# Kernel tuning notes

Measured on AMD Instinct MI355X. Metric: run time of the kernel, lower is better.

## Reference

```python
import jax, jax.numpy as jnp
import numpy as np

N_NODES = 50000
N_EDGES = 800000
D_IN = 128
D_HID = 128
D_OUT = 64
N_CONV = 4  # num_layers=5 -> 4 GINConv layers
BN_EPS = 1e-5


def setup_inputs() -> dict:
    key = jax.random.key(0)
    ks = jax.random.split(key, 16)
    h = jax.random.normal(ks[0], (N_NODES, D_IN), dtype=jnp.float32)
    src = jax.random.randint(ks[1], (N_EDGES,), 0, N_NODES)
    dst = jax.random.randint(ks[2], (N_EDGES,), 0, N_NODES)
    s = 0.05
    return {
        "h": h, "src": src, "dst": dst,
        # MLP inside each GINConv: Linear(no bias) -> BN -> ReLU -> Linear(no bias)
        "W1": jax.random.normal(ks[3], (N_CONV, D_IN, D_HID), dtype=jnp.float32) * s,
        "W2": jax.random.normal(ks[4], (N_CONV, D_HID, D_HID), dtype=jnp.float32) * s,
        "bn1_g": jnp.ones((N_CONV, D_HID), jnp.float32),
        "bn1_b": jnp.zeros((N_CONV, D_HID), jnp.float32),
        # outer BatchNorm after each GINConv
        "bn2_g": jnp.ones((N_CONV, D_HID), jnp.float32),
        "bn2_b": jnp.zeros((N_CONV, D_HID), jnp.float32),
        # 5 linear_prediction heads (layer 0 acts on input features)
        "pred_W": jax.random.normal(ks[5], (N_CONV + 1, D_HID, D_OUT), dtype=jnp.float32) * s,
        "pred_b": jnp.zeros((N_CONV + 1, D_OUT), jnp.float32),
    }


def _batchnorm(x, gamma, beta):
    # training-mode BatchNorm1d: batch statistics over the node dimension
    m = jnp.mean(x, axis=0)
    v = jnp.var(x, axis=0)
    return (x - m) * jax.lax.rsqrt(v + BN_EPS) * gamma + beta


def reference(h, src, dst, W1, W2, bn1_g, bn1_b, bn2_g, bn2_b, pred_W, pred_b):
    hidden_rep = [h]
    for i in range(N_CONV):
        # GINConv, learn_eps=False (eps=0): (1+eps)*h + sum of neighbor features
        agg = jax.ops.segment_sum(h[src], dst, num_segments=N_NODES)
        z = h + agg
        # MLP: Linear -> BN -> ReLU -> Linear
        z = z @ W1[i]
        z = jax.nn.relu(_batchnorm(z, bn1_g[i], bn1_b[i]))
        z = z @ W2[i]
        # outer BN + ReLU
        h = jax.nn.relu(_batchnorm(z, bn2_g[i], bn2_b[i]))
        hidden_rep.append(h)
    # SumPooling over the single graph, per-layer prediction heads (dropout = identity at eval)
    score = jnp.zeros((D_OUT,), h.dtype)
    for i, hr in enumerate(hidden_rep):
        pooled = jnp.sum(hr, axis=0)  # [D]
        score = score + pooled @ pred_W[i] + pred_b[i]
    return score  # [D_OUT], matches .view(shape[1])
```

## Files before the change

### kernel.cpp

```cpp
#include <hip/hip_runtime.h>
#include <hip/hip_bf16.h>

#define N_NODES 50000
#define N_EDGES 800000
#define D 128

typedef __bf16 bf16;
typedef __attribute__((ext_vector_type(8))) __bf16 bf16x8;
typedef __attribute__((ext_vector_type(4))) __bf16 bf16x4;
typedef __attribute__((ext_vector_type(16))) float f32x16;
typedef _Float16 f16;
typedef __attribute__((ext_vector_type(2))) _Float16 f16x2;
typedef __attribute__((ext_vector_type(4))) _Float16 f16x4;
typedef __attribute__((ext_vector_type(8))) _Float16 f16x8;

__global__ __launch_bounds__(256)
void initprep_kernel(const float* __restrict__ W1, const float* __restrict__ W2,
                     bf16* __restrict__ WfH, bf16* __restrict__ WfL,
                     int* __restrict__ deg, float* __restrict__ stats,
                     float* __restrict__ ppart, float* __restrict__ pooled,
                     int* __restrict__ done) {
    int b = blockIdx.x, t = threadIdx.x;
    if (b < 64) {
        int gid = b * 256 + t;
        int lane = gid & 63;
        int grp = gid >> 6;
        int sub = grp & 7;
        int cf = (grp >> 3) & 3;
        int m = grp >> 5;
        const float* Wsrc = (m < 4) ? (W1 + m * 16384) : (W2 + (m - 4) * 16384);
        int col = cf * 32 + (lane & 31);
        int kb = sub * 16 + 8 * (lane >> 5);
        bf16x8 h, l;
#pragma unroll
        for (int j = 0; j < 8; ++j) {
            float w = Wsrc[(kb + j) * 128 + col];
            bf16 hb = (bf16)w;
            bf16 lb = (bf16)(w - (float)hb);
            h[j] = hb;
            l[j] = lb;
        }
        int idx = m * 16384 + ((grp & 31) * 64 + lane) * 8;
        *(bf16x8*)&WfH[idx] = h;
        *(bf16x8*)&WfL[idx] = l;
    } else {
        int i = (b - 64) * 256 + t;
        if (i < N_NODES) deg[i] = 0;
        if (i < 2048) stats[i] = 0.f;
        if (i < 24576) ppart[i] = 0.f;
        if (i < 640) pooled[i] = 0.f;
        if (i < 2) done[i] = 0;
    }
}

__global__ void hist_kernel(const int* __restrict__ dst, int* __restrict__ deg) {
    int e = blockIdx.x * 256 + threadIdx.x;
    atomicAdd(&deg[dst[e]], 1);
}

__global__ __launch_bounds__(256)
void scanAB_kernel(const int* __restrict__ deg, int* __restrict__ bsum,
                   int* __restrict__ boff, int* __restrict__ done) {
    __shared__ int red[256];
    __shared__ int lastflag;
    int t = threadIdx.x;
    int g = blockIdx.x * 256 + t;
    red[t] = (g < N_NODES) ? deg[g] : 0;
    __syncthreads();
    for (int off = 128; off > 0; off >>= 1) {
        if (t < off) red[t] += red[t + off];
        __syncthreads();
    }
    if (t == 0) {
        __hip_atomic_store(&bsum[blockIdx.x], red[0], __ATOMIC_RELEASE,
                           __HIP_MEMORY_SCOPE_AGENT);
        __threadfence();
        int v = atomicAdd(&done[0], 1);
        lastflag = (v == (int)gridDim.x - 1);
    }
    __syncthreads();
    if (!lastflag) return;
    __shared__ int s[256];
    int v = (t < 196) ? __hip_atomic_load(&bsum[t], __ATOMIC_ACQUIRE,
                                          __HIP_MEMORY_SCOPE_AGENT)
                      : 0;
    s[t] = v;
    __syncthreads();
    for (int off = 1; off < 256; off <<= 1) {
        int a = (t >= off) ? s[t - off] : 0;
        __syncthreads();
        s[t] += a;
        __syncthreads();
    }
    boff[t] = (t == 0) ? 0 : s[t - 1];
}

__global__ __launch_bounds__(256)
void scanC_kernel(const int* __restrict__ deg, const int* __restrict__ boff,
                  int* __restrict__ row_start, int* __restrict__ cursor) {
    __shared__ int s[256];
    int t = threadIdx.x;
    int g = blockIdx.x * 256 + t;
    int v = (g < N_NODES) ? deg[g] : 0;
    s[t] = v;
    __syncthreads();
    for (int off = 1; off < 256; off <<= 1) {
        int a = (t >= off) ? s[t - off] : 0;
        __syncthreads();
        s[t] += a;
        __syncthreads();
    }
    int excl = boff[blockIdx.x] + s[t] - v;
    if (g < N_NODES) {
        row_start[g] = excl;
        cursor[g] = excl;
    }
    if (blockIdx.x == 0 && t == 0) row_start[N_NODES] = N_EDGES;
}

__global__ void fill_kernel(const int* __restrict__ src, const int* __restrict__ dst,
                            int* __restrict__ cursor, int* __restrict__ esrc) {
    int e = blockIdx.x * 256 + threadIdx.x;
    int d = dst[e];
    int p = atomicAdd(&cursor[d], 1);
    esrc[p] = src[e];
}

__global__ __launch_bounds__(256)
void conv0_kernel(const float* __restrict__ Y, f16* __restrict__ Hb,
                  float* __restrict__ pooled) {
    __shared__ float red[8][128];
    int t = threadIdx.x;
    int c = (t & 31) << 2;
    int rrow = t >> 5;
    float4 p = make_float4(0.f, 0.f, 0.f, 0.f);
    for (int r = blockIdx.x * 8 + rrow; r < N_NODES; r += gridDim.x * 8) {
        float4 v = *(const float4*)&Y[r * D + c];
        f16x4 h4;
        h4[0] = (f16)v.x; h4[1] = (f16)v.y; h4[2] = (f16)v.z; h4[3] = (f16)v.w;
        *(f16x4*)&Hb[r * D + c] = h4;
        p.x += v.x; p.y += v.y; p.z += v.z; p.w += v.w;
    }
    *(float4*)&red[rrow][c] = p;
    __syncthreads();
    if (t < 128) {
        float s = 0.f;
#pragma unroll
        for (int i = 0; i < 8; ++i) s += red[i][t];
        atomicAdd(&pooled[t], s);
    }
}

template <bool APPLY>
__global__ __launch_bounds__(256)
void agg_kernel(const f16* __restrict__ H, const int* __restrict__ esrc,
                const int* __restrict__ row_start, const float* __restrict__ stats,
                const float* __restrict__ gam, const float* __restrict__ bet,
                f16* __restrict__ Z, float* __restrict__ ppart) {
    __shared__ float sred[4][128];
    int wv = threadIdx.x >> 6;
    int v = blockIdx.x * 4 + wv;
    int lane = threadIdx.x & 63;
    int c2 = lane << 1;
    float a0 = 1.f, b0 = 0.f, a1 = 1.f, b1 = 0.f;
    if (APPLY) {
        float m0 = stats[c2] * (1.0f / N_NODES);
        float q0 = stats[128 + c2] * (1.0f / N_NODES);
        float g0 = gam[c2] * rsqrtf(q0 - m0 * m0 + 1e-5f);
        a0 = g0; b0 = bet[c2] - m0 * g0;
        float m1 = stats[c2 + 1] * (1.0f / N_NODES);
        float q1 = stats[128 + c2 + 1] * (1.0f / N_NODES);
        float g1 = gam[c2 + 1] * rsqrtf(q1 - m1 * m1 + 1e-5f);
        a1 = g1; b1 = bet[c2 + 1] - m1 * g1;
    }
    int beg = row_start[v], end_ = row_start[v + 1];
    f16x2 sv = *(const f16x2*)&H[v * D + c2];
    float ax = (float)sv[0], ay = (float)sv[1];
    if (APPLY) {
        ax = fmaxf(fmaf(a0, ax, b0), 0.f);
        ay = fmaxf(fmaf(a1, ay, b1), 0.f);
        sred[wv][c2] = ax;
        sred[wv][c2 + 1] = ay;
    }
    int e = beg;
    for (; e + 4 <= end_; e += 4) {
        int s0 = esrc[e], s1 = esrc[e + 1], s2 = esrc[e + 2], s3 = esrc[e + 3];
        f16x2 v0 = *(const f16x2*)&H[s0 * D + c2];
        f16x2 v1 = *(const f16x2*)&H[s1 * D + c2];
        f16x2 v2 = *(const f16x2*)&H[s2 * D + c2];
        f16x2 v3 = *(const f16x2*)&H[s3 * D + c2];
        if (APPLY) {
            ax += fmaxf(fmaf(a0, (float)v0[0], b0), 0.f) + fmaxf(fmaf(a0, (float)v1[0], b0), 0.f)
                + fmaxf(fmaf(a0, (float)v2[0], b0), 0.f) + fmaxf(fmaf(a0, (float)v3[0], b0), 0.f);
            ay += fmaxf(fmaf(a1, (float)v0[1], b1), 0.f) + fmaxf(fmaf(a1, (float)v1[1], b1), 0.f)
                + fmaxf(fmaf(a1, (float)v2[1], b1), 0.f) + fmaxf(fmaf(a1, (float)v3[1], b1), 0.f);
        } else {
            ax += (float)v0[0] + (float)v1[0] + (float)v2[0] + (float)v3[0];
            ay += (float)v0[1] + (float)v1[1] + (float)v2[1] + (float)v3[1];
        }
    }
    for (; e < end_; ++e) {
        int s0 = esrc[e];
        f16x2 v0 = *(const f16x2*)&H[s0 * D + c2];
        if (APPLY) {
            ax += fmaxf(fmaf(a0, (float)v0[0], b0), 0.f);
            ay += fmaxf(fmaf(a1, (float)v0[1], b1), 0.f);
        } else {
            ax += (float)v0[0];
            ay += (float)v0[1];
        }
    }
    f16x2 zv;
    zv[0] = (f16)ax;
    zv[1] = (f16)ay;
    *(f16x2*)&Z[v * D + c2] = zv;
    if (APPLY) {
        __syncthreads();
        int t = threadIdx.x;
        if (t < 128) {
            float s = sred[0][t] + sred[1][t] + sred[2][t] + sred[3][t];
            atomicAdd(&ppart[(blockIdx.x & 63) * 128 + t], s);
        }
    }
}

template <bool BN_IN>
__global__ __launch_bounds__(256, 2)
void mm_kernel(const f16* __restrict__ X, const bf16* __restrict__ WfH,
               const bf16* __restrict__ WfL, const float* __restrict__ stats_in,
               const float* __restrict__ gam, const float* __restrict__ bet,
               f16* __restrict__ Y, float* __restrict__ stats_out) {
    __shared__ bf16 Ah[4096];
    __shared__ bf16 Al[4096];
    __shared__ float ab[2][128];

    int t = threadIdx.x;
    int w = t >> 6, lane = t & 63;
    if (BN_IN && t < 128) {
        float s = stats_in[t] * (1.0f / N_NODES);
        float q = stats_in[128 + t] * (1.0f / N_NODES);
        float a = gam[t] * rsqrtf(q - s * s + 1e-5f);
        ab[0][t] = a;
        ab[1][t] = bet[t] - s * a;
    }

    bf16x8 Bh[8], Bl[8];
#pragma unroll
    for (int c = 0; c < 8; ++c) {
        int idx = ((w * 8 + c) * 64 + lane) * 8;
        Bh[c] = *(const bf16x8*)&WfH[idx];
        Bl[c] = *(const bf16x8*)&WfL[idx];
    }

    f32x16 acc[4];
#pragma unroll
    for (int fr = 0; fr < 4; ++fr) acc[fr] = (f32x16)0.0f;

    int rowbase = blockIdx.x * 128;
    int nrows = min(128, N_NODES - rowbase);
    int srow = t >> 1;
    int sk0 = (t & 1) * 16;
    __syncthreads();

    for (int kb = 0; kb < 4; ++kb) {
        if (kb) __syncthreads();
        {
            float vf[16];
#pragma unroll
            for (int j = 0; j < 16; ++j) vf[j] = 0.f;
            if (srow < nrows) {
                const f16* xr = &X[(rowbase + srow) * D + kb * 32 + sk0];
                f16x8 u0 = *(const f16x8*)&xr[0];
                f16x8 u1 = *(const f16x8*)&xr[8];
#pragma unroll
                for (int j = 0; j < 8; ++j) {
                    vf[j] = (float)u0[j];
                    vf[8 + j] = (float)u1[j];
                }
                if (BN_IN) {
#pragma unroll
                    for (int j = 0; j < 16; ++j) {
                        int kg = kb * 32 + sk0 + j;
                        vf[j] = fmaxf(fmaf(ab[0][kg], vf[j], ab[1][kg]), 0.f);
                    }
                }
            }
#pragma unroll
            for (int i = 0; i < 4; ++i) {
                bf16x4 h4, l4;
#pragma unroll
                for (int j = 0; j < 4; ++j) {
                    bf16 hb = (bf16)vf[i * 4 + j];
                    h4[j] = hb;
                    l4[j] = (bf16)(vf[i * 4 + j] - (float)hb);
                }
                int e = srow * 32 + sk0 + i * 4;
                int es = e ^ ((srow & 7) << 3);
                *(bf16x4*)&Ah[es] = h4;
                *(bf16x4*)&Al[es] = l4;
            }
        }
        __syncthreads();
#pragma unroll
        for (int s2 = 0; s2 < 2; ++s2) {
            int sg = kb * 2 + s2;
#pragma unroll
            for (int fr = 0; fr < 4; ++fr) {
                int row = fr * 32 + (lane & 31);
                int e = row * 32 + s2 * 16 + 8 * (lane >> 5);
                int es = e ^ ((row & 7) << 3);
                bf16x8 ah = *(const bf16x8*)&Ah[es];
                bf16x8 al = *(const bf16x8*)&Al[es];
                acc[fr] = __builtin_amdgcn_mfma_f32_32x32x16_bf16(al, Bh[sg], acc[fr], 0, 0, 0);
                acc[fr] = __builtin_amdgcn_mfma_f32_32x32x16_bf16(ah, Bl[sg], acc[fr], 0, 0, 0);
                acc[fr] = __builtin_amdgcn_mfma_f32_32x32x16_bf16(ah, Bh[sg], acc[fr], 0, 0, 0);
            }
        }
    }

    int col = w * 32 + (lane & 31);
    float psum = 0.f, psq = 0.f;
#pragma unroll
    for (int fr = 0; fr < 4; ++fr) {
#pragma unroll
        for (int r = 0; r < 16; ++r) {
            float v = acc[fr][r];
            int row = fr * 32 + (r & 3) + 8 * (r >> 2) + 4 * (lane >> 5);
            if (row < nrows) Y[(rowbase + row) * D + col] = (f16)v;
            psum += v;
            psq += v * v;
        }
    }
    psum += __shfl_xor(psum, 32);
    psq += __shfl_xor(psq, 32);
    if (lane < 32) {
        atomicAdd(&stats_out[col], psum);
        atomicAdd(&stats_out[128 + col], psq);
    }
}

__global__ __launch_bounds__(256)
void pool4head_kernel(const f16* __restrict__ Y, const float* __restrict__ stats,
                      const float* __restrict__ gam, const float* __restrict__ bet,
                      float* __restrict__ pooled, const float* __restrict__ ppart,
                      const float* __restrict__ pW, const float* __restrict__ pB,
                      float* __restrict__ out, int* __restrict__ done) {
    __shared__ float abS[2][128];
    __shared__ float red[8][128];
    __shared__ int lastflag;
    int t = threadIdx.x;
    if (t < 128) {
        float s = stats[t] * (1.0f / N_NODES);
        float q = stats[128 + t] * (1.0f / N_NODES);
        float a = gam[t] * rsqrtf(q - s * s + 1e-5f);
        abS[0][t] = a;
        abS[1][t] = bet[t] - s * a;
    }
    __syncthreads();
    int c = (t & 31) << 2;
    int rrow = t >> 5;
    float4 A = *(const float4*)&abS[0][c];
    float4 B = *(const float4*)&abS[1][c];
    float4 p = make_float4(0.f, 0.f, 0.f, 0.f);
    for (int r = blockIdx.x * 8 + rrow; r < N_NODES; r += gridDim.x * 8) {
        f16x4 v = *(const f16x4*)&Y[r * D + c];
        p.x += fmaxf(fmaf(A.x, (float)v[0], B.x), 0.f);
        p.y += fmaxf(fmaf(A.y, (float)v[1], B.y), 0.f);
        p.z += fmaxf(fmaf(A.z, (float)v[2], B.z), 0.f);
        p.w += fmaxf(fmaf(A.w, (float)v[3], B.w), 0.f);
    }
    *(float4*)&red[rrow][c] = p;
    __syncthreads();
    if (t < 128) {
        float s = 0.f;
#pragma unroll
        for (int i = 0; i < 8; ++i) s += red[i][t];
        atomicAdd(&pooled[512 + t], s);
    }
    __syncthreads();
    if (t == 0) {
        __threadfence();
        int v = atomicAdd(&done[1], 1);
        lastflag = (v == (int)gridDim.x - 1);
    }
    __syncthreads();
    if (!lastflag) return;

    __shared__ float pl[5][128];
    if (t < 128) {
        pl[0][t] = pooled[t];
        for (int l = 1; l <= 3; ++l) {
            float s = 0.f;
            for (int sl = 0; sl < 64; ++sl) s += ppart[(l - 1) * 8192 + sl * 128 + t];
            pl[l][t] = s;
        }
        pl[4][t] = __hip_atomic_load(&pooled[512 + t], __ATOMIC_ACQUIRE,
                                     __HIP_MEMORY_SCOPE_AGENT);
    }
    __syncthreads();
    if (t < 64) {
        float acc = 0.f;
        for (int l = 0; l < 5; ++l) {
            acc += pB[l * 64 + t];
            const float* wp = pW + l * 8192;
            const float* pp = pl[l];
            for (int cc = 0; cc < 128; ++cc) acc += pp[cc] * wp[cc * 64 + t];
        }
        out[t] = acc;
    }
}

extern "C" void kernel_launch(void* const* d_in, const int* in_sizes, int n_in,
                              void* d_out, int out_size, void* d_ws, size_t ws_size,
                              hipStream_t stream) {
    const float* h0 = (const float*)d_in[0];
    const int* src = (const int*)d_in[1];
    const int* dst = (const int*)d_in[2];
    const float* W1 = (const float*)d_in[3];
    const float* W2 = (const float*)d_in[4];
    const float* bn1_g = (const float*)d_in[5];
    const float* bn1_b = (const float*)d_in[6];
    const float* bn2_g = (const float*)d_in[7];
    const float* bn2_b = (const float*)d_in[8];
    const float* pW = (const float*)d_in[9];
    const float* pB = (const float*)d_in[10];
    float* out = (float*)d_out;

    char* ws = (char*)d_ws;
    f16* B0 = (f16*)(ws + 0);
    f16* B1 = (f16*)(ws + 12800000);
    f16* B2 = (f16*)(ws + 25600000);
    int* esrc = (int*)(ws + 38400000);
    int* deg = (int*)(ws + 54412288);
    int* row_start = (int*)(ws + 54612288);
    int* cursor = (int*)(ws + 54812304);
    int* done = (int*)(ws + 55012304);
    int* bsum = (int*)(ws + 55015440);
    int* boff = (int*)(ws + 55016224);
    float* stats = (float*)(ws + 55017248);
    float* ppart = (float*)(ws + 55025440);
    float* pooled = (float*)(ws + 55123744);
    bf16* WfH = (bf16*)(ws + 55126304);
    bf16* WfL = (bf16*)(ws + 55388448);

    initprep_kernel<<<260, 256, 0, stream>>>(W1, W2, WfH, WfL, deg, stats, ppart, pooled,
                                             done);
    hist_kernel<<<3125, 256, 0, stream>>>(dst, deg);
    scanAB_kernel<<<196, 256, 0, stream>>>(deg, bsum, boff, done);
    scanC_kernel<<<196, 256, 0, stream>>>(deg, boff, row_start, cursor);
    fill_kernel<<<3125, 256, 0, stream>>>(src, dst, cursor, esrc);
    conv0_kernel<<<512, 256, 0, stream>>>(h0, B0, pooled);

    for (int i = 0; i < 4; ++i) {
        if (i == 0) {
            agg_kernel<false><<<12500, 256, 0, stream>>>(B0, esrc, row_start, nullptr,
                                                         nullptr, nullptr, B1, nullptr);
        } else {
            agg_kernel<true><<<12500, 256, 0, stream>>>(
                B0, esrc, row_start, stats + (4 + i - 1) * 256, bn2_g + (i - 1) * 128,
                bn2_b + (i - 1) * 128, B1, ppart + (i - 1) * 8192);
        }
        mm_kernel<false><<<391, 256, 0, stream>>>(B1, WfH + i * 16384, WfL + i * 16384,
                                                  nullptr, nullptr, nullptr, B2,
                                                  stats + i * 256);
        mm_kernel<true><<<391, 256, 0, stream>>>(B2, WfH + (4 + i) * 16384,
                                                 WfL + (4 + i) * 16384, stats + i * 256,
                                                 bn1_g + i * 128, bn1_b + i * 128, B0,
                                                 stats + (4 + i) * 256);
    }
    pool4head_kernel<<<512, 256, 0, stream>>>(B0, stats + 7 * 256, bn2_g + 3 * 128,
                                              bn2_b + 3 * 128, pooled, ppart, pW, pB, out,
                                              done);
}
```

Before: 594.2 us.

## Fuse conv0 into init, single-pass lookback scan, parallelize pooling head

Moves the fp32-to-fp16 input conversion into the init kernel and folds layer-0 pooling into the first aggregation kernel. The two-kernel degree scan is replaced by a single-pass scan where each block spins on predecessor flags. The final pooled-partial reduction is spread over several blocks and the prediction-head matvec uses all 256 threads. The aim is fewer launches and a shorter serial tail, at the risk of spin-wait dependence on block residency.

```diff
diff --git a/kernel.cpp b/kernel.cpp
--- a/kernel.cpp
+++ b/kernel.cpp
@@ -18,8 +18,10 @@
 void initprep_kernel(const float* __restrict__ W1, const float* __restrict__ W2,
                      bf16* __restrict__ WfH, bf16* __restrict__ WfL,
                      int* __restrict__ deg, float* __restrict__ stats,
-                     float* __restrict__ ppart, float* __restrict__ pooled,
-                     int* __restrict__ done) {
+                     float* __restrict__ ppart, float* __restrict__ plglob,
+                     float* __restrict__ pooled4, int* __restrict__ done,
+                     int* __restrict__ flags, const float* __restrict__ h0,
+                     f16* __restrict__ Hb) {
     int b = blockIdx.x, t = threadIdx.x;
     if (b < 64) {
         int gid = b * 256 + t;
@@ -43,13 +45,24 @@
         int idx = m * 16384 + ((grp & 31) * 64 + lane) * 8;
         *(bf16x8*)&WfH[idx] = h;
         *(bf16x8*)&WfL[idx] = l;
-    } else {
+    } else if (b < 260) {
         int i = (b - 64) * 256 + t;
         if (i < N_NODES) deg[i] = 0;
         if (i < 2048) stats[i] = 0.f;
-        if (i < 24576) ppart[i] = 0.f;
-        if (i < 640) pooled[i] = 0.f;
+        if (i < 32768) ppart[i] = 0.f;
+        if (i < 512) plglob[i] = 0.f;
+        if (i < 128) pooled4[i] = 0.f;
         if (i < 2) done[i] = 0;
+        if (i < 196) flags[i] = 0;
+    } else {
+        int c = (t & 31) << 2;
+        int rrow = t >> 5;
+        for (int r = (b - 260) * 8 + rrow; r < N_NODES; r += 512 * 8) {
+            float4 v = *(const float4*)&h0[r * D + c];
+            f16x4 h4;
+            h4[0] = (f16)v.x; h4[1] = (f16)v.y; h4[2] = (f16)v.z; h4[3] = (f16)v.w;
+            *(f16x4*)&Hb[r * D + c] = h4;
+        }
     }
 }
 
@@ -59,31 +72,14 @@
 }
 
 __global__ __launch_bounds__(256)
-void scanAB_kernel(const int* __restrict__ deg, int* __restrict__ bsum,
-                   int* __restrict__ boff, int* __restrict__ done) {
-    __shared__ int red[256];
-    __shared__ int lastflag;
-    int t = threadIdx.x;
-    int g = blockIdx.x * 256 + t;
-    red[t] = (g < N_NODES) ? deg[g] : 0;
-    __syncthreads();
-    for (int off = 128; off > 0; off >>= 1) {
-        if (t < off) red[t] += red[t + off];
-        __syncthreads();
-    }
-    if (t == 0) {
-        __hip_atomic_store(&bsum[blockIdx.x], red[0], __ATOMIC_RELEASE,
-                           __HIP_MEMORY_SCOPE_AGENT);
-        __threadfence();
-        int v = atomicAdd(&done[0], 1);
-        lastflag = (v == (int)gridDim.x - 1);
-    }
-    __syncthreads();
-    if (!lastflag) return;
+void scan_kernel(const int* __restrict__ deg, int* __restrict__ bsum,
+                 int* __restrict__ flags, int* __restrict__ row_start,
+                 int* __restrict__ cursor) {
     __shared__ int s[256];
-    int v = (t < 196) ? __hip_atomic_load(&bsum[t], __ATOMIC_ACQUIRE,
-                                          __HIP_MEMORY_SCOPE_AGENT)
-                      : 0;
+    __shared__ int rsum[256];
+    int t = threadIdx.x, b = blockIdx.x;
+    int g = b * 256 + t;
+    int v = (g < N_NODES) ? deg[g] : 0;
     s[t] = v;
     __syncthreads();
     for (int off = 1; off < 256; off <<= 1) {
@@ -92,30 +88,27 @@
         s[t] += a;
         __syncthreads();
     }
-    boff[t] = (t == 0) ? 0 : s[t - 1];
-}
-
-__global__ __launch_bounds__(256)
-void scanC_kernel(const int* __restrict__ deg, const int* __restrict__ boff,
-                  int* __restrict__ row_start, int* __restrict__ cursor) {
-    __shared__ int s[256];
-    int t = threadIdx.x;
-    int g = blockIdx.x * 256 + t;
-    int v = (g < N_NODES) ? deg[g] : 0;
-    s[t] = v;
-    __syncthreads();
-    for (int off = 1; off < 256; off <<= 1) {
-        int a = (t >= off) ? s[t - off] : 0;
+    if (t == 0) {
+        __hip_atomic_store(&bsum[b], s[255], __ATOMIC_RELEASE, __HIP_MEMORY_SCOPE_AGENT);
+        __hip_atomic_store(&flags[b], 1, __ATOMIC_RELEASE, __HIP_MEMORY_SCOPE_AGENT);
+    }
+    int part = 0;
+    for (int j = t; j < b; j += 256) {
+        while (__hip_atomic_load(&flags[j], __ATOMIC_ACQUIRE, __HIP_MEMORY_SCOPE_AGENT) == 0) {}
+        part += __hip_atomic_load(&bsum[j], __ATOMIC_ACQUIRE, __HIP_MEMORY_SCOPE_AGENT);
+    }
+    rsum[t] = part;
+    __syncthreads();
+    for (int off = 128; off > 0; off >>= 1) {
+        if (t < off) rsum[t] += rsum[t + off];
         __syncthreads();
-        s[t] += a;
-        __syncthreads();
-    }
-    int excl = boff[blockIdx.x] + s[t] - v;
+    }
+    int excl = rsum[0] + s[t] - v;
     if (g < N_NODES) {
         row_start[g] = excl;
         cursor[g] = excl;
     }
-    if (blockIdx.x == 0 && t == 0) row_start[N_NODES] = N_EDGES;
+    if (b == 0 && t == 0) row_start[N_NODES] = N_EDGES;
 }
 
 __global__ void fill_kernel(const int* __restrict__ src, const int* __restrict__ dst,
@@ -124,31 +117,6 @@
     int d = dst[e];
     int p = atomicAdd(&cursor[d], 1);
     esrc[p] = src[e];
-}
-
-__global__ __launch_bounds__(256)
-void conv0_kernel(const float* __restrict__ Y, f16* __restrict__ Hb,
-                  float* __restrict__ pooled) {
-    __shared__ float red[8][128];
-    int t = threadIdx.x;
-    int c = (t & 31) << 2;
-    int rrow = t >> 5;
-    float4 p = make_float4(0.f, 0.f, 0.f, 0.f);
-    for (int r = blockIdx.x * 8 + rrow; r < N_NODES; r += gridDim.x * 8) {
-        float4 v = *(const float4*)&Y[r * D + c];
-        f16x4 h4;
-        h4[0] = (f16)v.x; h4[1] = (f16)v.y; h4[2] = (f16)v.z; h4[3] = (f16)v.w;
-        *(f16x4*)&Hb[r * D + c] = h4;
-        p.x += v.x; p.y += v.y; p.z += v.z; p.w += v.w;
-    }
-    *(float4*)&red[rrow][c] = p;
-    __syncthreads();
-    if (t < 128) {
-        float s = 0.f;
-#pragma unroll
-        for (int i = 0; i < 8; ++i) s += red[i][t];
-        atomicAdd(&pooled[t], s);
-    }
 }
 
 template <bool APPLY>
@@ -179,9 +147,9 @@
     if (APPLY) {
         ax = fmaxf(fmaf(a0, ax, b0), 0.f);
         ay = fmaxf(fmaf(a1, ay, b1), 0.f);
-        sred[wv][c2] = ax;
-        sred[wv][c2 + 1] = ay;
-    }
+    }
+    sred[wv][c2] = ax;
+    sred[wv][c2 + 1] = ay;
     int e = beg;
     for (; e + 4 <= end_; e += 4) {
         int s0 = esrc[e], s1 = esrc[e + 1], s2 = esrc[e + 2], s3 = esrc[e + 3];
@@ -214,13 +182,11 @@
     zv[0] = (f16)ax;
     zv[1] = (f16)ay;
     *(f16x2*)&Z[v * D + c2] = zv;
-    if (APPLY) {
-        __syncthreads();
-        int t = threadIdx.x;
-        if (t < 128) {
-            float s = sred[0][t] + sred[1][t] + sred[2][t] + sred[3][t];
-            atomicAdd(&ppart[(blockIdx.x & 63) * 128 + t], s);
-        }
+    __syncthreads();
+    int t = threadIdx.x;
+    if (t < 128) {
+        float s = sred[0][t] + sred[1][t] + sred[2][t] + sred[3][t];
+        atomicAdd(&ppart[(blockIdx.x & 63) * 128 + t], s);
     }
 }
 
@@ -342,13 +308,23 @@
 __global__ __launch_bounds__(256)
 void pool4head_kernel(const f16* __restrict__ Y, const float* __restrict__ stats,
                       const float* __restrict__ gam, const float* __restrict__ bet,
-                      float* __restrict__ pooled, const float* __restrict__ ppart,
-                      const float* __restrict__ pW, const float* __restrict__ pB,
-                      float* __restrict__ out, int* __restrict__ done) {
+                      const float* __restrict__ ppart, float* __restrict__ plglob,
+                      float* __restrict__ pooled4, const float* __restrict__ pW,
+                      const float* __restrict__ pB, float* __restrict__ out,
+                      int* __restrict__ done) {
     __shared__ float abS[2][128];
     __shared__ float red[8][128];
     __shared__ int lastflag;
-    int t = threadIdx.x;
+    int t = threadIdx.x, b = blockIdx.x;
+
+    if (b < 4 && t < 128) {
+        float s = 0.f;
+#pragma unroll
+        for (int sl = 0; sl < 64; ++sl) s += ppart[b * 8192 + sl * 128 + t];
+        __hip_atomic_store(&plglob[b * 128 + t], s, __ATOMIC_RELEASE,
+                           __HIP_MEMORY_SCOPE_AGENT);
+    }
+
     if (t < 128) {
         float s = stats[t] * (1.0f / N_NODES);
         float q = stats[128 + t] * (1.0f / N_NODES);
@@ -362,7 +338,7 @@
     float4 A = *(const float4*)&abS[0][c];
     float4 B = *(const float4*)&abS[1][c];
     float4 p = make_float4(0.f, 0.f, 0.f, 0.f);
-    for (int r = blockIdx.x * 8 + rrow; r < N_NODES; r += gridDim.x * 8) {
+    for (int r = b * 8 + rrow; r < N_NODES; r += gridDim.x * 8) {
         f16x4 v = *(const f16x4*)&Y[r * D + c];
         p.x += fmaxf(fmaf(A.x, (float)v[0], B.x), 0.f);
         p.y += fmaxf(fmaf(A.y, (float)v[1], B.y), 0.f);
@@ -375,7 +351,7 @@
         float s = 0.f;
 #pragma unroll
         for (int i = 0; i < 8; ++i) s += red[i][t];
-        atomicAdd(&pooled[512 + t], s);
+        atomicAdd(&pooled4[t], s);
     }
     __syncthreads();
     if (t == 0) {
@@ -387,26 +363,36 @@
     if (!lastflag) return;
 
     __shared__ float pl[5][128];
+    __shared__ float red2[4][64];
     if (t < 128) {
-        pl[0][t] = pooled[t];
-        for (int l = 1; l <= 3; ++l) {
-            float s = 0.f;
-            for (int sl = 0; sl < 64; ++sl) s += ppart[(l - 1) * 8192 + sl * 128 + t];
-            pl[l][t] = s;
-        }
-        pl[4][t] = __hip_atomic_load(&pooled[512 + t], __ATOMIC_ACQUIRE,
+#pragma unroll
+        for (int l = 0; l < 4; ++l)
+            pl[l][t] = __hip_atomic_load(&plglob[l * 128 + t], __ATOMIC_ACQUIRE,
+                                         __HIP_MEMORY_SCOPE_AGENT);
+        pl[4][t] = __hip_atomic_load(&pooled4[t], __ATOMIC_ACQUIRE,
                                      __HIP_MEMORY_SCOPE_AGENT);
     }
     __syncthreads();
+    int o = t & 63, q = t >> 6;
+    float acc0 = 0.f, acc1 = 0.f;
+#pragma unroll
+    for (int l = 0; l < 5; ++l) {
+        const float* wp = pW + l * 8192;
+#pragma unroll
+        for (int cc = 0; cc < 16; ++cc) {
+            int c0 = q * 32 + cc;
+            int c1 = q * 32 + 16 + cc;
+            acc0 += pl[l][c0] * wp[c0 * 64 + o];
+            acc1 += pl[l][c1] * wp[c1 * 64 + o];
+        }
+    }
+    red2[q][o] = acc0 + acc1;
+    __syncthreads();
     if (t < 64) {
-        float acc = 0.f;
-        for (int l = 0; l < 5; ++l) {
-            acc += pB[l * 64 + t];
-            const float* wp = pW + l * 8192;
-            const float* pp = pl[l];
-            for (int cc = 0; cc < 128; ++cc) acc += pp[cc] * wp[cc * 64 + t];
-        }
-        out[t] = acc;
+        float s = red2[0][t] + red2[1][t] + red2[2][t] + red2[3][t];
+#pragma unroll
+        for (int l = 0; l < 5; ++l) s += pB[l * 64 + t];
+        out[t] = s;
     }
 }
 
@@ -431,34 +417,33 @@
     f16* B1 = (f16*)(ws + 12800000);
     f16* B2 = (f16*)(ws + 25600000);
     int* esrc = (int*)(ws + 38400000);
-    int* deg = (int*)(ws + 54412288);
-    int* row_start = (int*)(ws + 54612288);
-    int* cursor = (int*)(ws + 54812304);
-    int* done = (int*)(ws + 55012304);
-    int* bsum = (int*)(ws + 55015440);
-    int* boff = (int*)(ws + 55016224);
-    float* stats = (float*)(ws + 55017248);
-    float* ppart = (float*)(ws + 55025440);
-    float* pooled = (float*)(ws + 55123744);
-    bf16* WfH = (bf16*)(ws + 55126304);
-    bf16* WfL = (bf16*)(ws + 55388448);
-
-    initprep_kernel<<<260, 256, 0, stream>>>(W1, W2, WfH, WfL, deg, stats, ppart, pooled,
-                                             done);
+    int* deg = (int*)(ws + 41600000);
+    int* row_start = (int*)(ws + 41800000);
+    int* cursor = (int*)(ws + 42000016);
+    int* bsum = (int*)(ws + 42200016);
+    int* flags = (int*)(ws + 42200800);
+    int* done = (int*)(ws + 42201600);
+    float* stats = (float*)(ws + 42201664);
+    float* ppart = (float*)(ws + 42209856);
+    float* plglob = (float*)(ws + 42340928);
+    float* pooled4 = (float*)(ws + 42342976);
+    bf16* WfH = (bf16*)(ws + 42343488);
+    bf16* WfL = (bf16*)(ws + 42605632);
+
+    initprep_kernel<<<772, 256, 0, stream>>>(W1, W2, WfH, WfL, deg, stats, ppart, plglob,
+                                             pooled4, done, flags, h0, B0);
     hist_kernel<<<3125, 256, 0, stream>>>(dst, deg);
-    scanAB_kernel<<<196, 256, 0, stream>>>(deg, bsum, boff, done);
-    scanC_kernel<<<196, 256, 0, stream>>>(deg, boff, row_start, cursor);
+    scan_kernel<<<196, 256, 0, stream>>>(deg, bsum, flags, row_start, cursor);
     fill_kernel<<<3125, 256, 0, stream>>>(src, dst, cursor, esrc);
-    conv0_kernel<<<512, 256, 0, stream>>>(h0, B0, pooled);
 
     for (int i = 0; i < 4; ++i) {
         if (i == 0) {
             agg_kernel<false><<<12500, 256, 0, stream>>>(B0, esrc, row_start, nullptr,
-                                                         nullptr, nullptr, B1, nullptr);
+                                                         nullptr, nullptr, B1, ppart);
         } else {
             agg_kernel<true><<<12500, 256, 0, stream>>>(
                 B0, esrc, row_start, stats + (4 + i - 1) * 256, bn2_g + (i - 1) * 128,
-                bn2_b + (i - 1) * 128, B1, ppart + (i - 1) * 8192);
+                bn2_b + (i - 1) * 128, B1, ppart + i * 8192);
         }
         mm_kernel<false><<<391, 256, 0, stream>>>(B1, WfH + i * 16384, WfL + i * 16384,
                                                   nullptr, nullptr, nullptr, B2,
@@ -469,6 +454,6 @@
                                                  stats + (4 + i) * 256);
     }
     pool4head_kernel<<<512, 256, 0, stream>>>(B0, stats + 7 * 256, bn2_g + 3 * 128,
-                                              bn2_b + 3 * 128, pooled, ppart, pW, pB, out,
-                                              done);
-}
+                                              bn2_b + 3 * 128, ppart, plglob, pooled4, pW,
+                                              pB, out, done);
+}
```

New measurement: 542.8 us. 8.7% less time.
